# Performance work log

Hardware: AMD Instinct MI355X
Metric: run time of the kernel (lower is better)

## Reference

```python
import jax, jax.numpy as jnp
import numpy as np

N_CHANNELS = 29
HIDDEN = [5, 4, 4]
IN_FEAT = 7
OUT_FEAT = 3
EPS = 1e-07


def _glorot(key, fan_in, fan_out, shape):
    lim = np.sqrt(6.0 / (fan_in + fan_out))
    return jax.random.uniform(key, shape, jnp.float32, -lim, lim)


def _make_params(key):
    # Batched per-channel weights: stack n_channels tiny MLPs along leading dim.
    sizes = [IN_FEAT] + HIDDEN + [OUT_FEAT]
    Ws, bs = [], []
    for i in range(len(sizes) - 1):
        key, k = jax.random.split(key)
        Ws.append(_glorot(k, sizes[i], sizes[i + 1], (N_CHANNELS, sizes[i], sizes[i + 1])))
        bs.append(jnp.zeros((N_CHANNELS, sizes[i + 1]), jnp.float32))
    return Ws, bs


def setup_inputs() -> dict:
    key = jax.random.key(0)
    ks = jax.random.split(key, 16)
    N = 262144
    inp = {
        "tau": jax.random.uniform(ks[0], (N, N_CHANNELS, 1), jnp.float32),
        "mu": jax.random.uniform(ks[1], (N, 1), jnp.float32, 0.05, 1.0),
        "mu_bar": jax.random.uniform(ks[2], (N, 1), jnp.float32, 0.05, 1.0),
        "lw": jax.random.uniform(ks[3], (N, 1), jnp.float32),
        "h2o": jax.random.uniform(ks[4], (N, 1), jnp.float32),
        "o3": jax.random.uniform(ks[5], (N, 1), jnp.float32),
        "co2": jax.random.uniform(ks[6], (N, 1), jnp.float32),
        "u": jax.random.uniform(ks[7], (N, 1), jnp.float32),
        "n2o": jax.random.uniform(ks[8], (N, 1), jnp.float32),
        "ch4": jax.random.uniform(ks[9], (N, 1), jnp.float32),
    }
    Wd, bd = _make_params(ks[10])
    Wf, bf = _make_params(ks[11])
    for i in range(4):
        inp[f"Wd{i}"] = Wd[i]
        inp[f"bd{i}"] = bd[i]
        inp[f"Wf{i}"] = Wf[i]
        inp[f"bf{i}"] = bf[i]
    return inp


def _mlp(x, Ws, bs):
    # x: [N, F]; Ws[i]: [C, fin, fout]; output [N, C, 3]
    h = jnp.einsum('nf,cfh->nch', x, Ws[0]) + bs[0]
    h = jax.nn.relu(h)
    for i in (1, 2):
        h = jnp.einsum('nch,chk->nck', h, Ws[i]) + bs[i]
        h = jax.nn.relu(h)
    h = jnp.einsum('nch,chk->nck', h, Ws[3]) + bs[3]
    return jax.nn.softmax(h, axis=-1)


def reference(tau, mu, mu_bar, lw, h2o, o3, co2, u, n2o, ch4,
              Wd0, bd0, Wd1, bd1, Wd2, bd2, Wd3, bd3,
              Wf0, bf0, Wf1, bf1, Wf2, bf2, Wf3, bf3):
    constituents = jnp.concatenate([lw, h2o, o3, co2, u, n2o, ch4], axis=1)  # [N,7]
    c_direct = constituents / (mu + EPS)
    c_diffuse = constituents / (mu_bar + EPS)
    mu3 = mu[:, :, None]          # [N,1,1]
    mu_bar3 = mu_bar[:, :, None]
    tau_total = jnp.sum(tau, axis=-1, keepdims=True)  # [N,C,1]
    t_direct = jnp.exp(-tau_total / (mu3 + EPS))       # [N,C,1]
    t_diffuse = jnp.exp(-tau_total / (mu_bar3 + EPS))
    e_direct = _mlp(c_direct, [Wd0, Wd1, Wd2, Wd3], [bd0, bd1, bd2, bd3])    # [N,C,3]
    e_diffuse = _mlp(c_diffuse, [Wf0, Wf1, Wf2, Wf3], [bf0, bf1, bf2, bf3])  # [N,C,3]
    return jnp.concatenate([t_direct, t_diffuse, e_direct, e_diffuse], axis=2)  # [N,C,8]
```

## Files before the change

### kernel.cpp

```cpp
#include <hip/hip_runtime.h>

#define EPS 1e-7f
#define NCH 29
#define SPB 128
#define ROWA 17


typedef float f32x2 __attribute__((ext_vector_type(2)));
typedef float nf4   __attribute__((ext_vector_type(4)));

__device__ __forceinline__ f32x2 splat2(float v) { f32x2 r; r.x = v; r.y = v; return r; }
__device__ __forceinline__ f32x2 fma2(f32x2 a, f32x2 b, f32x2 c) {
    return __builtin_elementwise_fma(a, b, c);
}
__device__ __forceinline__ f32x2 max2(f32x2 a, f32x2 b) {
    return __builtin_elementwise_max(a, b);
}
__device__ __forceinline__ f32x2 expc2(f32x2 a) {
    f32x2 r; r.x = __expf(a.x); r.y = __expf(a.y); return r;
}
__device__ __forceinline__ f32x2 rcp2(f32x2 a) {
    f32x2 r; r.x = __builtin_amdgcn_rcpf(a.x); r.y = __builtin_amdgcn_rcpf(a.y); return r;
}
__device__ __forceinline__ nf4 mk4(float a, float b, float c, float d) {
    nf4 r; r.x = a; r.y = b; r.z = c; r.w = d; return r;
}

__device__ __forceinline__ void barrier_lds_only() {
    asm volatile("s_waitcnt lgkmcnt(0)\n\ts_barrier" ::: "memory");
}

__device__ __forceinline__ void mlp7p(const f32x2 x[7],
    const float* __restrict__ W0, const float* __restrict__ b0,
    const float* __restrict__ W1, const float* __restrict__ b1,
    const float* __restrict__ W2, const float* __restrict__ b2,
    const float* __restrict__ W3, const float* __restrict__ b3,
    f32x2 e[3])
{
    const f32x2 zero = splat2(0.0f);
    f32x2 h0[5];
#pragma unroll
    for (int h = 0; h < 5; ++h) {
        f32x2 a = splat2(b0[h]);
#pragma unroll
        for (int f = 0; f < 7; ++f) a = fma2(x[f], splat2(W0[f * 5 + h]), a);
        h0[h] = max2(a, zero);
    }
    f32x2 h1[4];
#pragma unroll
    for (int k = 0; k < 4; ++k) {
        f32x2 a = splat2(b1[k]);
#pragma unroll
        for (int h = 0; h < 5; ++h) a = fma2(h0[h], splat2(W1[h * 4 + k]), a);
        h1[k] = max2(a, zero);
    }
    f32x2 h2[4];
#pragma unroll
    for (int k = 0; k < 4; ++k) {
        f32x2 a = splat2(b2[k]);
#pragma unroll
        for (int h = 0; h < 4; ++h) a = fma2(h1[h], splat2(W2[h * 4 + k]), a);
        h2[k] = max2(a, zero);
    }
    f32x2 l[3];
#pragma unroll
    for (int k = 0; k < 3; ++k) {
        f32x2 a = splat2(b3[k]);
#pragma unroll
        for (int h = 0; h < 4; ++h) a = fma2(h2[h], splat2(W3[h * 3 + k]), a);
        l[k] = a;
    }
    f32x2 m = max2(l[0], max2(l[1], l[2]));
    f32x2 e0 = expc2(l[0] - m);
    f32x2 e1 = expc2(l[1] - m);
    f32x2 e2 = expc2(l[2] - m);
    f32x2 rs = rcp2(e0 + e1 + e2);
    e[0] = e0 * rs; e[1] = e1 * rs; e[2] = e2 * rs;
}

__global__ __launch_bounds__(256, 4) void lps_kernel(
    const float* __restrict__ tau, const float* __restrict__ mu, const float* __restrict__ mu_bar,
    const float* __restrict__ lw, const float* __restrict__ h2o, const float* __restrict__ o3,
    const float* __restrict__ co2, const float* __restrict__ uu, const float* __restrict__ n2o,
    const float* __restrict__ ch4,
    const float* __restrict__ Wd0, const float* __restrict__ bd0,
    const float* __restrict__ Wf0, const float* __restrict__ bf0,
    const float* __restrict__ Wd1, const float* __restrict__ bd1,
    const float* __restrict__ Wf1, const float* __restrict__ bf1,
    const float* __restrict__ Wd2, const float* __restrict__ bd2,
    const float* __restrict__ Wf2, const float* __restrict__ bf2,
    const float* __restrict__ Wd3, const float* __restrict__ bd3,
    const float* __restrict__ Wf3, const float* __restrict__ bf3,
    float* __restrict__ out, int N)
{
    __shared__ __align__(16) nf4 obuf[SPB * ROWA];

    const int tid  = threadIdx.x;
    const int lane = tid & 63;
    const int wid  = __builtin_amdgcn_readfirstlane(tid >> 6);

    const long long base = (long long)blockIdx.x * SPB;
    const int s0 = (int)base + lane;
    const int s1 = s0 + 64;
    const int i0 = (s0 < N) ? s0 : (N - 1);
    const int i1 = (s1 < N) ? s1 : (N - 1);

    f32x2 mu2, mub2;
    mu2.x  = mu[i0];      mu2.y  = mu[i1];
    mub2.x = mu_bar[i0];  mub2.y = mu_bar[i1];
    const f32x2 rmu2  = rcp2(mu2 + splat2(EPS));
    const f32x2 rmub2 = rcp2(mub2 + splat2(EPS));

    f32x2 cons2[7];
    cons2[0].x = lw[i0];  cons2[0].y = lw[i1];
    cons2[1].x = h2o[i0]; cons2[1].y = h2o[i1];
    cons2[2].x = o3[i0];  cons2[2].y = o3[i1];
    cons2[3].x = co2[i0]; cons2[3].y = co2[i1];
    cons2[4].x = uu[i0];  cons2[4].y = uu[i1];
    cons2[5].x = n2o[i0]; cons2[5].y = n2o[i1];
    cons2[6].x = ch4[i0]; cons2[6].y = ch4[i1];

    f32x2 tauv1[4], tauv2[4];
#pragma unroll
    for (int k = 0; k < 4; ++k) {
        const int c1 = k * 8 + wid;
        const int c2 = c1 + 4;
        const int cc2 = (c2 < NCH) ? c2 : 0;
        tauv1[k].x = tau[(size_t)i0 * NCH + c1];
        tauv1[k].y = tau[(size_t)i1 * NCH + c1];
        tauv2[k].x = tau[(size_t)i0 * NCH + cc2];
        tauv2[k].y = tau[(size_t)i1 * NCH + cc2];
    }

    int nsamp = N - (int)base;
    if (nsamp > SPB) nsamp = SPB;
    nf4* out4 = (nf4*)out;

#pragma unroll
    for (int k = 0; k < 4; ++k) {
#pragma unroll
        for (int v = 0; v < 2; ++v) {
            const int c = k * 8 + wid + v * 4;
            if (c < NCH) {
                const f32x2 tt = v ? tauv2[k] : tauv1[k];
                const f32x2 td2 = expc2(-(tt * rmu2));
                const f32x2 tf2 = expc2(-(tt * rmub2));

                f32x2 x2[7];
                f32x2 ed[3], ef[3];
#pragma unroll
                for (int f = 0; f < 7; ++f) x2[f] = cons2[f] * rmu2;
                mlp7p(x2, Wd0 + c * 35, bd0 + c * 5, Wd1 + c * 20, bd1 + c * 4,
                          Wd2 + c * 16, bd2 + c * 4, Wd3 + c * 12, bd3 + c * 3, ed);
#pragma unroll
                for (int f = 0; f < 7; ++f) x2[f] = cons2[f] * rmub2;
                mlp7p(x2, Wf0 + c * 35, bf0 + c * 5, Wf1 + c * 20, bf1 + c * 4,
                          Wf2 + c * 16, bf2 + c * 4, Wf3 + c * 12, bf3 + c * 3, ef);

                const int r = (c - k * 8) * 2;
                obuf[lane * ROWA + r]            = mk4(td2.x, tf2.x, ed[0].x, ed[1].x);
                obuf[lane * ROWA + r + 1]        = mk4(ed[2].x, ef[0].x, ef[1].x, ef[2].x);
                obuf[(lane + 64) * ROWA + r]     = mk4(td2.y, tf2.y, ed[0].y, ed[1].y);
                obuf[(lane + 64) * ROWA + r + 1] = mk4(ed[2].y, ef[0].y, ef[1].y, ef[2].y);
            }
        }

        barrier_lds_only();

        if (nsamp > 0) {
            if (k < 3) {
                const int tot = nsamp * 16;
                for (int i = tid; i < tot; i += 256) {
                    const int s = i >> 4, rr = i & 15;
                    out4[(base + s) * 58 + k * 16 + rr] = obuf[s * ROWA + rr];
                }
            } else {
                const int tot = nsamp * 10;
                for (int i = tid; i < tot; i += 256) {
                    const int s = i / 10, rr = i - s * 10;
                    out4[(base + s) * 58 + 48 + rr] = obuf[s * ROWA + rr];
                }
            }
        }

        barrier_lds_only();
    }
}

extern "C" void kernel_launch(void* const* d_in, const int* in_sizes, int n_in,
                              void* d_out, int out_size, void* d_ws, size_t ws_size,
                              hipStream_t stream) {
    const float* tau    = (const float*)d_in[0];
    const float* mu     = (const float*)d_in[1];
    const float* mu_bar = (const float*)d_in[2];
    const float* lw     = (const float*)d_in[3];
    const float* h2o    = (const float*)d_in[4];
    const float* o3     = (const float*)d_in[5];
    const float* co2    = (const float*)d_in[6];
    const float* uu     = (const float*)d_in[7];
    const float* n2o    = (const float*)d_in[8];
    const float* ch4    = (const float*)d_in[9];

    const float* Wd0 = (const float*)d_in[10];
    const float* bd0 = (const float*)d_in[11];
    const float* Wf0 = (const float*)d_in[12];
    const float* bf0 = (const float*)d_in[13];
    const float* Wd1 = (const float*)d_in[14];
    const float* bd1 = (const float*)d_in[15];
    const float* Wf1 = (const float*)d_in[16];
    const float* bf1 = (const float*)d_in[17];
    const float* Wd2 = (const float*)d_in[18];
    const float* bd2 = (const float*)d_in[19];
    const float* Wf2 = (const float*)d_in[20];
    const float* bf2 = (const float*)d_in[21];
    const float* Wd3 = (const float*)d_in[22];
    const float* bd3 = (const float*)d_in[23];
    const float* Wf3 = (const float*)d_in[24];
    const float* bf3 = (const float*)d_in[25];

    float* out = (float*)d_out;
    int N = in_sizes[1];

    int blocks = (N + SPB - 1) / SPB;
    lps_kernel<<<blocks, 256, 0, stream>>>(
        tau, mu, mu_bar, lw, h2o, o3, co2, uu, n2o, ch4,
        Wd0, bd0, Wf0, bf0, Wd1, bd1, Wf1, bf1,
        Wd2, bd2, Wf2, bf2, Wd3, bd3, Wf3, bf3,
        out, N);
}
```

Measured before the change: 80.58 us.

## Give each wavefront its own samples and channels loop, dropping block barriers

Work is reassigned so that each wavefront handles 128 samples across all 29 channels, two channels per step, instead of splitting channels across the four waves of a block. Every wave stages its outputs in a private LDS slice and writes them out straight away, which removes the block-wide barriers. Tau loads are software-prefetched two steps ahead. The trade-offs are more per-thread weight loads, since the channel index is now uniform across the wave, and smaller global store chunks per step (64 bytes per sample), which may hurt write coalescing. Intra-wave LDS ordering is relied on without an explicit wait.

Measured after the change: 179.9 us. 123% more time.

```diff
diff --git a/kernel.cpp b/kernel.cpp
--- a/kernel.cpp
+++ b/kernel.cpp
@@ -2,8 +2,9 @@
 
 #define EPS 1e-7f
 #define NCH 29
-#define SPB 128
-#define ROWA 17
+#define SPW 128
+#define SPB 512
+#define NCK 15
 
 
 typedef float f32x2 __attribute__((ext_vector_type(2)));
@@ -24,10 +25,6 @@
 }
 __device__ __forceinline__ nf4 mk4(float a, float b, float c, float d) {
     nf4 r; r.x = a; r.y = b; r.z = c; r.w = d; return r;
-}
-
-__device__ __forceinline__ void barrier_lds_only() {
-    asm volatile("s_waitcnt lgkmcnt(0)\n\ts_barrier" ::: "memory");
 }
 
 __device__ __forceinline__ void mlp7p(const f32x2 x[7],
@@ -93,14 +90,14 @@
     const float* __restrict__ Wf3, const float* __restrict__ bf3,
     float* __restrict__ out, int N)
 {
-    __shared__ __align__(16) nf4 obuf[SPB * ROWA];
+    __shared__ __align__(16) nf4 obuf[4][4 * SPW];
 
     const int tid  = threadIdx.x;
     const int lane = tid & 63;
     const int wid  = __builtin_amdgcn_readfirstlane(tid >> 6);
 
-    const long long base = (long long)blockIdx.x * SPB;
-    const int s0 = (int)base + lane;
+    const long long wsbase = (long long)blockIdx.x * SPB + (long long)wid * SPW;
+    const int s0 = (int)wsbase + lane;
     const int s1 = s0 + 64;
     const int i0 = (s0 < N) ? s0 : (N - 1);
     const int i1 = (s1 < N) ? s1 : (N - 1);
@@ -120,29 +117,37 @@
     cons2[5].x = n2o[i0]; cons2[5].y = n2o[i1];
     cons2[6].x = ch4[i0]; cons2[6].y = ch4[i1];
 
-    f32x2 tauv1[4], tauv2[4];
-#pragma unroll
-    for (int k = 0; k < 4; ++k) {
-        const int c1 = k * 8 + wid;
-        const int c2 = c1 + 4;
-        const int cc2 = (c2 < NCH) ? c2 : 0;
-        tauv1[k].x = tau[(size_t)i0 * NCH + c1];
-        tauv1[k].y = tau[(size_t)i1 * NCH + c1];
-        tauv2[k].x = tau[(size_t)i0 * NCH + cc2];
-        tauv2[k].y = tau[(size_t)i1 * NCH + cc2];
-    }
-
-    int nsamp = N - (int)base;
-    if (nsamp > SPB) nsamp = SPB;
-    nf4* out4 = (nf4*)out;
-
-#pragma unroll
-    for (int k = 0; k < 4; ++k) {
+    int wsamp = N - (int)wsbase;
+    if (wsamp > SPW) wsamp = SPW;
+    if (wsamp < 0)  wsamp = 0;
+
+    nf4* const ob   = &obuf[wid][0];
+    nf4* const out4 = (nf4*)out;
+    const float* taub = tau;
+
+    f32x2 tA[NCK], tB[NCK];
+#pragma unroll
+    for (int k = 0; k < 2; ++k) {
+        const int c0 = 2 * k, c1 = 2 * k + 1;
+        tA[k].x = taub[(size_t)i0 * NCH + c0]; tA[k].y = taub[(size_t)i1 * NCH + c0];
+        tB[k].x = taub[(size_t)i0 * NCH + c1]; tB[k].y = taub[(size_t)i1 * NCH + c1];
+    }
+
+#pragma unroll
+    for (int k = 0; k < NCK; ++k) {
+        if (k + 2 < NCK) {
+            const int c0 = 2 * (k + 2), c1 = c0 + 1;
+            tA[k + 2].x = taub[(size_t)i0 * NCH + c0];
+            tA[k + 2].y = taub[(size_t)i1 * NCH + c0];
+            tB[k + 2].x = taub[(size_t)i0 * NCH + c1];
+            tB[k + 2].y = taub[(size_t)i1 * NCH + c1];
+        }
+
 #pragma unroll
         for (int v = 0; v < 2; ++v) {
-            const int c = k * 8 + wid + v * 4;
+            const int c = 2 * k + v;
             if (c < NCH) {
-                const f32x2 tt = v ? tauv2[k] : tauv1[k];
+                const f32x2 tt = v ? tB[k] : tA[k];
                 const f32x2 td2 = expc2(-(tt * rmu2));
                 const f32x2 tf2 = expc2(-(tt * rmub2));
 
@@ -157,33 +162,28 @@
                 mlp7p(x2, Wf0 + c * 35, bf0 + c * 5, Wf1 + c * 20, bf1 + c * 4,
                           Wf2 + c * 16, bf2 + c * 4, Wf3 + c * 12, bf3 + c * 3, ef);
 
-                const int r = (c - k * 8) * 2;
-                obuf[lane * ROWA + r]            = mk4(td2.x, tf2.x, ed[0].x, ed[1].x);
-                obuf[lane * ROWA + r + 1]        = mk4(ed[2].x, ef[0].x, ef[1].x, ef[2].x);
-                obuf[(lane + 64) * ROWA + r]     = mk4(td2.y, tf2.y, ed[0].y, ed[1].y);
-                obuf[(lane + 64) * ROWA + r + 1] = mk4(ed[2].y, ef[0].y, ef[1].y, ef[2].y);
+                const int r = v * 2;
+                ob[r * SPW + lane]            = mk4(td2.x, tf2.x, ed[0].x, ed[1].x);
+                ob[(r + 1) * SPW + lane]      = mk4(ed[2].x, ef[0].x, ef[1].x, ef[2].x);
+                ob[r * SPW + lane + 64]       = mk4(td2.y, tf2.y, ed[0].y, ed[1].y);
+                ob[(r + 1) * SPW + lane + 64] = mk4(ed[2].y, ef[0].y, ef[1].y, ef[2].y);
             }
         }
 
-        barrier_lds_only();
-
-        if (nsamp > 0) {
-            if (k < 3) {
-                const int tot = nsamp * 16;
-                for (int i = tid; i < tot; i += 256) {
-                    const int s = i >> 4, rr = i & 15;
-                    out4[(base + s) * 58 + k * 16 + rr] = obuf[s * ROWA + rr];
-                }
-            } else {
-                const int tot = nsamp * 10;
-                for (int i = tid; i < tot; i += 256) {
-                    const int s = i / 10, rr = i - s * 10;
-                    out4[(base + s) * 58 + 48 + rr] = obuf[s * ROWA + rr];
+        {
+            const int cnt = (k < NCK - 1) ? 4 : 2;
+#pragma unroll
+            for (int i2 = 0; i2 < 8; ++i2) {
+                const int i = lane + i2 * 64;
+                if (i < SPW * cnt) {
+                    const int s  = (cnt == 4) ? (i >> 2) : (i >> 1);
+                    const int rr = (cnt == 4) ? (i & 3) : (i & 1);
+                    if (s < wsamp) {
+                        out4[(wsbase + s) * 58 + k * 4 + rr] = ob[rr * SPW + s];
+                    }
                 }
             }
         }
-
-        barrier_lds_only();
     }
 }
 
```
